# Kernel tuning notes

Hardware: AMD Instinct MI355X
Metric: run time of the kernel (lower is better)

Reference implementation:

```python
import jax, jax.numpy as jnp
import numpy as np

HID = (128, 256, 128)  # nmp_qc NNet hidden layer sizes
D_IN = 256
TARGET = 256


def _mlp_params(key, n_in, n_out, prefix):
    sizes = (n_in,) + HID + (n_out,)
    params = {}
    for i in range(len(sizes) - 1):
        key, k1, k2 = jax.random.split(key, 3)
        fan_in = sizes[i]
        bound = 1.0 / np.sqrt(fan_in)
        params[f"{prefix}_W{i}"] = jax.random.uniform(k1, (sizes[i], sizes[i + 1]), jnp.float32, -bound, bound)
        params[f"{prefix}_b{i}"] = jax.random.uniform(k2, (sizes[i + 1],), jnp.float32, -bound, bound)
    return params, key


def _mlp(x, Ws, bs):
    # ReLU on all layers except the last (linear output), matching NNet
    for i in range(len(Ws) - 1):
        x = jax.nn.relu(x @ Ws[i] + bs[i])
    return x @ Ws[-1] + bs[-1]


def setup_inputs() -> dict:
    key = jax.random.key(0)
    k0, k1, key = jax.random.split(key, 3)
    B, N = 512, 256
    inp = {
        "h0": jax.random.normal(k0, (B, N, D_IN), jnp.float32),
        "hT": jax.random.normal(k1, (B, N, D_IN), jnp.float32),
    }
    gp, key = _mlp_params(key, 2 * D_IN, TARGET, "g")  # gate MLP: concat(h0,hT) -> target
    op, key = _mlp_params(key, D_IN, TARGET, "o")      # value MLP: hT -> target
    inp.update(gp)
    inp.update(op)
    return inp


def reference(h0, hT,
              g_W0, g_b0, g_W1, g_b1, g_W2, g_b2, g_W3, g_b3,
              o_W0, o_b0, o_W1, o_b1, o_W2, o_b2, o_W3, o_b3):
    gWs = (g_W0, g_W1, g_W2, g_W3)
    gbs = (g_b0, g_b1, g_b2, g_b3)
    oWs = (o_W0, o_W1, o_W2, o_W3)
    obs = (o_b0, o_b1, o_b2, o_b3)
    # gate: sigmoid(MLP1([h0; hT])) ; value: MLP2(hT)  -- all [B, N, target]
    gate = jax.nn.sigmoid(_mlp(jnp.concatenate([h0, hT], axis=-1), gWs, gbs))
    val = _mlp(hT, oWs, obs)
    # node validity mask: sum of initial features > 0, matching r_mpnn
    mask = (jnp.sum(h0, axis=-1, keepdims=True) > 0).astype(h0.dtype)  # [B, N, 1]
    return jnp.sum(mask * gate * val, axis=1)  # [B, target]
```

## Files before the change

### kernel.cpp

```cpp
#include <hip/hip_runtime.h>
#include <hip/hip_bf16.h>
#include <stdint.h>


typedef __attribute__((ext_vector_type(8))) short short8_t;
typedef __attribute__((ext_vector_type(16))) float f32x16;

#define ROWS 64
#define NWG  2048

#define PE        (64 * 136)
#define OFF_P     0
#define OFF_A     34816
#define OFF_MASK  52224
#define LDS_TOTAL 52480

__device__ __forceinline__ short f2bf(float f) {
  union { float f; uint32_t u; } v; v.f = f;
  uint32_t r = (v.u + 0x7FFFu + ((v.u >> 16) & 1u)) >> 16;
  return (short)r;
}
__device__ __forceinline__ float bf2f(short b) {
  union { uint32_t u; float f; } v; v.u = ((uint32_t)(uint16_t)b) << 16;
  return v.f;
}

template <int KT16, int KSTEPS, int CT>
__device__ __forceinline__ void gemm32(const short* actin, int Sin,
                                       const short* __restrict__ wsB, int ks0, int cb0,
                                       f32x16 (&acc)[2][CT], int lane) {
  const int n32 = lane & 31, q32 = lane >> 5;
#pragma unroll
  for (int ks = 0; ks < KSTEPS; ++ks) {
    const int kl = ks * 16 + q32 * 8;
    short8_t b[CT];
#pragma unroll
    for (int ct = 0; ct < CT; ++ct)
      b[ct] = *(const short8_t*)(wsB + (((cb0 + ct) * KT16 + ks0 + ks) << 9) + lane * 8);
    short8_t a[2];
#pragma unroll
    for (int rt = 0; rt < 2; ++rt)
      a[rt] = *(const short8_t*)(actin + (rt * 32 + n32) * Sin + kl);
#pragma unroll
    for (int ct = 0; ct < CT; ++ct)
#pragma unroll
      for (int rt = 0; rt < 2; ++rt)
        acc[rt][ct] = __builtin_amdgcn_mfma_f32_32x32x16_bf16(a[rt], b[ct], acc[rt][ct], 0, 0, 0);
  }
}

template <int CT, int ACTF>
__device__ __forceinline__ void epi32(f32x16 (&acc)[2][CT], short* actout, int Sout,
                                      const float* __restrict__ bias, int c0, int n32, int q32) {
#pragma unroll
  for (int ct = 0; ct < CT; ++ct) {
    const int c = c0 + ct * 32 + n32;
    const float bv = bias[c];
#pragma unroll
    for (int rt = 0; rt < 2; ++rt)
#pragma unroll
      for (int reg = 0; reg < 16; ++reg) {
        const int r = rt * 32 + (reg & 3) + 8 * (reg >> 2) + 4 * q32;
        float v = acc[rt][ct][reg] + bv;
        if (ACTF == 1) v = fmaxf(v, 0.f);
        actout[r * Sout + c] = f2bf(v);
      }
  }
}

template <int K, int N, int ACTF>
__device__ __forceinline__ void layer32(const short* actin, int Sin, short* actout, int Sout,
                                        const short* __restrict__ wsB,
                                        const float* __restrict__ bias,
                                        int wv, int lane) {
  constexpr int CT = N / 128;
  const int cb0 = wv * CT;
  const int n32 = lane & 31, q32 = lane >> 5;
  f32x16 acc[2][CT];
#pragma unroll
  for (int rt = 0; rt < 2; ++rt)
#pragma unroll
    for (int ct = 0; ct < CT; ++ct) acc[rt][ct] = (f32x16)(0.f);
  gemm32<K / 16, K / 16, CT>(actin, Sin, wsB, 0, cb0, acc, lane);
  epi32<CT, ACTF>(acc, actout, Sout, bias, cb0 * 32, n32, q32);
}

__device__ __forceinline__ void stage_load(const float* __restrict__ src, int row0, int colbase,
                                           int tid, float4 (&v)[8]) {
  const int c4 = tid & 31, rb = tid >> 5;
#pragma unroll
  for (int it = 0; it < 8; ++it)
    v[it] = *(const float4*)(src + (size_t)(row0 + rb + it * 8) * 256 + colbase + c4 * 4);
}

__device__ __forceinline__ void stage_store(short* Pb, int tid, const float4 (&v)[8],
                                            float* maskacc, int mmode) {
  const int c4 = tid & 31, rb = tid >> 5;
#pragma unroll
  for (int it = 0; it < 8; ++it) {
    const int r = rb + it * 8;
    short4 pk; pk.x = f2bf(v[it].x); pk.y = f2bf(v[it].y); pk.z = f2bf(v[it].z); pk.w = f2bf(v[it].w);
    *(short4*)(Pb + r * 136 + c4 * 4) = pk;
    if (mmode) {
      float s = v[it].x + v[it].y + v[it].z + v[it].w;
      s += __shfl_down(s, 16, 32);
      s += __shfl_down(s, 8, 32);
      s += __shfl_down(s, 4, 32);
      s += __shfl_down(s, 2, 32);
      s += __shfl_down(s, 1, 32);
      if (c4 == 0) {
        if (mmode == 1) maskacc[r] = s; else maskacc[r] += s;
      }
    }
  }
}

template <int NCH, bool MASKA>
__device__ __forceinline__ void stream32(const float* __restrict__ src0,
                                         const float* __restrict__ src1, int splitc,
                                         const short* __restrict__ wsB,
                                         const float* __restrict__ bias,
                                         short* P, short* Aout, float* maskacc,
                                         int row0, int tid, int wv, int lane) {
  constexpr int KT16 = NCH * 8;
  const int n32 = lane & 31, q32 = lane >> 5;
  f32x16 acc[2][1];
  acc[0][0] = (f32x16)(0.f); acc[1][0] = (f32x16)(0.f);
  float4 v[8];
  stage_load(src0, row0, 0, tid, v);
  stage_store(P, tid, v, maskacc, MASKA ? 1 : 0);
  __syncthreads();
#pragma unroll
  for (int kc = 0; kc < NCH; ++kc) {
    if (kc + 1 < NCH) {
      const bool lo = (kc + 1 < splitc);
      stage_load(lo ? src0 : src1, row0, (lo ? kc + 1 : kc + 1 - splitc) * 128, tid, v);
    }
    gemm32<KT16, 8, 1>(P + (kc & 1) * PE, 136, wsB, kc * 8, wv, acc, lane);
    if (kc + 1 < NCH)
      stage_store(P + ((kc + 1) & 1) * PE, tid, v, maskacc, (MASKA && kc + 1 < splitc) ? 2 : 0);
    __syncthreads();
  }
  epi32<1, 1>(acc, Aout, 136, bias, wv * 32, n32, q32);
}

__device__ __forceinline__ void gate_layer(const short* actin, const short* __restrict__ wsB,
                                           const float* __restrict__ bias,
                                           uint32_t (&gate)[2][2][8],
                                           int wv, int lane) {
  const int n32 = lane & 31;
  f32x16 acc[2][2];
#pragma unroll
  for (int rt = 0; rt < 2; ++rt)
#pragma unroll
    for (int ct = 0; ct < 2; ++ct) acc[rt][ct] = (f32x16)(0.f);
  gemm32<8, 8, 2>(actin, 136, wsB, 0, wv * 2, acc, lane);
#pragma unroll
  for (int ct = 0; ct < 2; ++ct) {
    const float bv = bias[wv * 64 + ct * 32 + n32];
#pragma unroll
    for (int rt = 0; rt < 2; ++rt)
#pragma unroll
      for (int p = 0; p < 8; ++p) {
        const float g0 = 1.f / (1.f + __expf(-(acc[rt][ct][2 * p] + bv)));
        const float g1 = 1.f / (1.f + __expf(-(acc[rt][ct][2 * p + 1] + bv)));
        gate[rt][ct][p] = ((uint32_t)(uint16_t)f2bf(g1) << 16) | (uint32_t)(uint16_t)f2bf(g0);
      }
  }
}

__device__ __forceinline__ void final32(const short* actin, const short* __restrict__ wsB,
                                        const float* __restrict__ bias,
                                        const uint32_t (&gate)[2][2][8],
                                        const float* maskacc, float* __restrict__ out,
                                        int row0, int wv, int lane) {
  const int n32 = lane & 31, q32 = lane >> 5;
  f32x16 acc[2][2];
#pragma unroll
  for (int rt = 0; rt < 2; ++rt)
#pragma unroll
    for (int ct = 0; ct < 2; ++ct) acc[rt][ct] = (f32x16)(0.f);
  gemm32<8, 8, 2>(actin, 136, wsB, 0, wv * 2, acc, lane);

  const int b = row0 >> 8;
#pragma unroll
  for (int ct = 0; ct < 2; ++ct) {
    const int c = wv * 64 + ct * 32 + n32;
    const float bv = bias[c];
    float s = 0.f;
#pragma unroll
    for (int rt = 0; rt < 2; ++rt)
#pragma unroll
      for (int p = 0; p < 8; ++p) {
        const int r0 = rt * 32 + ((2 * p) & 3) + 8 * (p >> 1) + 4 * q32;
        const float g0 = bf2f((short)(gate[rt][ct][p] & 0xFFFF));
        const float g1 = bf2f((short)(gate[rt][ct][p] >> 16));
        const float v0 = acc[rt][ct][2 * p] + bv;
        const float v1 = acc[rt][ct][2 * p + 1] + bv;
        if (maskacc[r0] > 0.f)     s += g0 * v0;
        if (maskacc[r0 + 1] > 0.f) s += g1 * v1;
      }
    s += __shfl_down(s, 32);
    if (lane < 32) atomicAdd(out + b * 256 + c, s);
  }
}

__global__ __launch_bounds__(256, 2)
void readout_main(const float* __restrict__ h0, const float* __restrict__ hT,
                  const short* __restrict__ ws,
                  const float* __restrict__ gb0, const float* __restrict__ gb1,
                  const float* __restrict__ gb2, const float* __restrict__ gb3,
                  const float* __restrict__ ob0, const float* __restrict__ ob1,
                  const float* __restrict__ ob2, const float* __restrict__ ob3,
                  float* __restrict__ out) {
  __shared__ __align__(16) char smem[LDS_TOTAL];
  short* P  = (short*)(smem + OFF_P);
  short* B2 = (short*)(smem + OFF_P);
  short* A  = (short*)(smem + OFF_A);
  float* maskacc = (float*)(smem + OFF_MASK);

  const int tid = threadIdx.x, lane = tid & 63, wv = tid >> 6;
  const int row0 = blockIdx.x * ROWS;
  uint32_t gate[2][2][8];

  stream32<4, true>(h0, hT, 2, ws + 0, gb0, P, A, maskacc, row0, tid, wv, lane);
  __syncthreads();
  layer32<128, 256, 1>(A, 136, B2, 264, ws + 65536, gb1, wv, lane);
  __syncthreads();
  layer32<256, 128, 1>(B2, 264, A, 136, ws + 98304, gb2, wv, lane);
  __syncthreads();
  gate_layer(A, ws + 131072, gb3, gate, wv, lane);
  __syncthreads();
  stream32<2, false>(hT, hT, 2, ws + 163840, ob0, P, A, maskacc, row0, tid, wv, lane);
  __syncthreads();
  layer32<128, 256, 1>(A, 136, B2, 264, ws + 196608, ob1, wv, lane);
  __syncthreads();
  layer32<256, 128, 1>(B2, 264, A, 136, ws + 229376, ob2, wv, lane);
  __syncthreads();
  final32(A, ws + 262144, ob3, gate, maskacc, out, row0, wv, lane);
}

__global__ void prep(const float* __restrict__ W0, const float* __restrict__ W1,
                     const float* __restrict__ W2, const float* __restrict__ W3,
                     const float* __restrict__ W4, const float* __restrict__ W5,
                     const float* __restrict__ W6, const float* __restrict__ W7,
                     short* __restrict__ ws, float* __restrict__ out) {
  const int l = blockIdx.y;
  const int le = blockIdx.x * 256 + threadIdx.x;
  if (l == 1) { out[le] = 0.f; out[le + 65536] = 0.f; }
  int K, N, off; const float* W;
  switch (l) {
    case 0:  K = 512; N = 128; off = 0;      W = W0; break;
    case 1:  K = 128; N = 256; off = 65536;  W = W1; break;
    case 2:  K = 256; N = 128; off = 98304;  W = W2; break;
    case 3:  K = 128; N = 256; off = 131072; W = W3; break;
    case 4:  K = 256; N = 128; off = 163840; W = W4; break;
    case 5:  K = 128; N = 256; off = 196608; W = W5; break;
    case 6:  K = 256; N = 128; off = 229376; W = W6; break;
    default: K = 128; N = 256; off = 262144; W = W7; break;
  }
  if (le >= K * N) return;
  const int j = le & 7;
  const int lanei = (le >> 3) & 63;
  const int blk = le >> 9;
  const int kt16 = K >> 4;
  const int ks = blk % kt16, cb = blk / kt16;
  const int n = cb * 32 + (lanei & 31);
  const int k = ks * 16 + (lanei >> 5) * 8 + j;
  ws[off + le] = f2bf(W[k * N + n]);
}

extern "C" void kernel_launch(void* const* d_in, const int* in_sizes, int n_in,
                              void* d_out, int out_size, void* d_ws, size_t ws_size,
                              hipStream_t stream) {
  const float* h0  = (const float*)d_in[0];
  const float* hT  = (const float*)d_in[1];
  const float* gW0 = (const float*)d_in[2];  const float* gb0 = (const float*)d_in[3];
  const float* gW1 = (const float*)d_in[4];  const float* gb1 = (const float*)d_in[5];
  const float* gW2 = (const float*)d_in[6];  const float* gb2 = (const float*)d_in[7];
  const float* gW3 = (const float*)d_in[8];  const float* gb3 = (const float*)d_in[9];
  const float* oW0 = (const float*)d_in[10]; const float* ob0 = (const float*)d_in[11];
  const float* oW1 = (const float*)d_in[12]; const float* ob1 = (const float*)d_in[13];
  const float* oW2 = (const float*)d_in[14]; const float* ob2 = (const float*)d_in[15];
  const float* oW3 = (const float*)d_in[16]; const float* ob3 = (const float*)d_in[17];
  float* out = (float*)d_out;
  short* ws  = (short*)d_ws;

  prep<<<dim3(256, 8), 256, 0, stream>>>(gW0, gW1, gW2, gW3, oW0, oW1, oW2, oW3, ws, out);
  readout_main<<<NWG, 256, 0, stream>>>(h0, hT, ws,
                                        gb0, gb1, gb2, gb3,
                                        ob0, ob1, ob2, ob3, out);
}
```

Before: 468.7 us.

## Split workgroup rows across 8 waves instead of 4

Doubles the threads per workgroup from 256 to 512, so each wave handles one 32-row tile instead of two while keeping the same column split. Streaming loads are spread over twice as many threads, and the launch bounds target more waves per CU to improve latency hiding. In exchange, each B-fragment weight load is now reused across one row tile instead of two, which doubles weight traffic per MFMA. The LDS footprint per 512-thread workgroup limits how many workgroups can be resident on a CU.

```diff
diff --git a/kernel.cpp b/kernel.cpp
--- a/kernel.cpp
+++ b/kernel.cpp
@@ -8,6 +8,7 @@
 
 #define ROWS 64
 #define NWG  2048
+#define NTHR 512
 
 #define PE        (64 * 136)
 #define OFF_P     0
@@ -28,7 +29,7 @@
 template <int KT16, int KSTEPS, int CT>
 __device__ __forceinline__ void gemm32(const short* actin, int Sin,
                                        const short* __restrict__ wsB, int ks0, int cb0,
-                                       f32x16 (&acc)[2][CT], int lane) {
+                                       f32x16 (&acc)[CT], int lane) {
   const int n32 = lane & 31, q32 = lane >> 5;
 #pragma unroll
   for (int ks = 0; ks < KSTEPS; ++ks) {
@@ -37,34 +38,27 @@
 #pragma unroll
     for (int ct = 0; ct < CT; ++ct)
       b[ct] = *(const short8_t*)(wsB + (((cb0 + ct) * KT16 + ks0 + ks) << 9) + lane * 8);
-    short8_t a[2];
-#pragma unroll
-    for (int rt = 0; rt < 2; ++rt)
-      a[rt] = *(const short8_t*)(actin + (rt * 32 + n32) * Sin + kl);
+    const short8_t a = *(const short8_t*)(actin + n32 * Sin + kl);
 #pragma unroll
     for (int ct = 0; ct < CT; ++ct)
-#pragma unroll
-      for (int rt = 0; rt < 2; ++rt)
-        acc[rt][ct] = __builtin_amdgcn_mfma_f32_32x32x16_bf16(a[rt], b[ct], acc[rt][ct], 0, 0, 0);
+      acc[ct] = __builtin_amdgcn_mfma_f32_32x32x16_bf16(a, b[ct], acc[ct], 0, 0, 0);
   }
 }
 
 template <int CT, int ACTF>
-__device__ __forceinline__ void epi32(f32x16 (&acc)[2][CT], short* actout, int Sout,
+__device__ __forceinline__ void epi32(f32x16 (&acc)[CT], short* actout, int Sout,
                                       const float* __restrict__ bias, int c0, int n32, int q32) {
 #pragma unroll
   for (int ct = 0; ct < CT; ++ct) {
     const int c = c0 + ct * 32 + n32;
     const float bv = bias[c];
 #pragma unroll
-    for (int rt = 0; rt < 2; ++rt)
-#pragma unroll
-      for (int reg = 0; reg < 16; ++reg) {
-        const int r = rt * 32 + (reg & 3) + 8 * (reg >> 2) + 4 * q32;
-        float v = acc[rt][ct][reg] + bv;
-        if (ACTF == 1) v = fmaxf(v, 0.f);
-        actout[r * Sout + c] = f2bf(v);
-      }
+    for (int reg = 0; reg < 16; ++reg) {
+      const int r = (reg & 3) + 8 * (reg >> 2) + 4 * q32;
+      float v = acc[ct][reg] + bv;
+      if (ACTF == 1) v = fmaxf(v, 0.f);
+      actout[r * Sout + c] = f2bf(v);
+    }
   }
 }
 
@@ -72,33 +66,31 @@
 __device__ __forceinline__ void layer32(const short* actin, int Sin, short* actout, int Sout,
                                         const short* __restrict__ wsB,
                                         const float* __restrict__ bias,
-                                        int wv, int lane) {
+                                        int wq, int lane) {
   constexpr int CT = N / 128;
-  const int cb0 = wv * CT;
-  const int n32 = lane & 31, q32 = lane >> 5;
-  f32x16 acc[2][CT];
-#pragma unroll
-  for (int rt = 0; rt < 2; ++rt)
-#pragma unroll
-    for (int ct = 0; ct < CT; ++ct) acc[rt][ct] = (f32x16)(0.f);
+  const int cb0 = wq * CT;
+  const int n32 = lane & 31, q32 = lane >> 5;
+  f32x16 acc[CT];
+#pragma unroll
+  for (int ct = 0; ct < CT; ++ct) acc[ct] = (f32x16)(0.f);
   gemm32<K / 16, K / 16, CT>(actin, Sin, wsB, 0, cb0, acc, lane);
   epi32<CT, ACTF>(acc, actout, Sout, bias, cb0 * 32, n32, q32);
 }
 
 __device__ __forceinline__ void stage_load(const float* __restrict__ src, int row0, int colbase,
-                                           int tid, float4 (&v)[8]) {
+                                           int tid, float4 (&v)[4]) {
   const int c4 = tid & 31, rb = tid >> 5;
 #pragma unroll
-  for (int it = 0; it < 8; ++it)
-    v[it] = *(const float4*)(src + (size_t)(row0 + rb + it * 8) * 256 + colbase + c4 * 4);
-}
-
-__device__ __forceinline__ void stage_store(short* Pb, int tid, const float4 (&v)[8],
+  for (int it = 0; it < 4; ++it)
+    v[it] = *(const float4*)(src + (size_t)(row0 + rb + it * 16) * 256 + colbase + c4 * 4);
+}
+
+__device__ __forceinline__ void stage_store(short* Pb, int tid, const float4 (&v)[4],
                                             float* maskacc, int mmode) {
   const int c4 = tid & 31, rb = tid >> 5;
 #pragma unroll
-  for (int it = 0; it < 8; ++it) {
-    const int r = rb + it * 8;
+  for (int it = 0; it < 4; ++it) {
+    const int r = rb + it * 16;
     short4 pk; pk.x = f2bf(v[it].x); pk.y = f2bf(v[it].y); pk.z = f2bf(v[it].z); pk.w = f2bf(v[it].w);
     *(short4*)(Pb + r * 136 + c4 * 4) = pk;
     if (mmode) {
@@ -121,12 +113,12 @@
                                          const short* __restrict__ wsB,
                                          const float* __restrict__ bias,
                                          short* P, short* Aout, float* maskacc,
-                                         int row0, int tid, int wv, int lane) {
+                                         int row0, int tid, int wq, int rowsh, int lane) {
   constexpr int KT16 = NCH * 8;
   const int n32 = lane & 31, q32 = lane >> 5;
-  f32x16 acc[2][1];
-  acc[0][0] = (f32x16)(0.f); acc[1][0] = (f32x16)(0.f);
-  float4 v[8];
+  f32x16 acc[1];
+  acc[0] = (f32x16)(0.f);
+  float4 v[4];
   stage_load(src0, row0, 0, tid, v);
   stage_store(P, tid, v, maskacc, MASKA ? 1 : 0);
   __syncthreads();
@@ -136,76 +128,66 @@
       const bool lo = (kc + 1 < splitc);
       stage_load(lo ? src0 : src1, row0, (lo ? kc + 1 : kc + 1 - splitc) * 128, tid, v);
     }
-    gemm32<KT16, 8, 1>(P + (kc & 1) * PE, 136, wsB, kc * 8, wv, acc, lane);
+    gemm32<KT16, 8, 1>(P + (kc & 1) * PE + rowsh, 136, wsB, kc * 8, wq, acc, lane);
     if (kc + 1 < NCH)
       stage_store(P + ((kc + 1) & 1) * PE, tid, v, maskacc, (MASKA && kc + 1 < splitc) ? 2 : 0);
     __syncthreads();
   }
-  epi32<1, 1>(acc, Aout, 136, bias, wv * 32, n32, q32);
+  epi32<1, 1>(acc, Aout, 136, bias, wq * 32, n32, q32);
 }
 
 __device__ __forceinline__ void gate_layer(const short* actin, const short* __restrict__ wsB,
                                            const float* __restrict__ bias,
-                                           uint32_t (&gate)[2][2][8],
-                                           int wv, int lane) {
+                                           uint32_t (&gate)[2][8],
+                                           int wq, int lane) {
   const int n32 = lane & 31;
-  f32x16 acc[2][2];
-#pragma unroll
-  for (int rt = 0; rt < 2; ++rt)
-#pragma unroll
-    for (int ct = 0; ct < 2; ++ct) acc[rt][ct] = (f32x16)(0.f);
-  gemm32<8, 8, 2>(actin, 136, wsB, 0, wv * 2, acc, lane);
+  f32x16 acc[2];
+  acc[0] = (f32x16)(0.f); acc[1] = (f32x16)(0.f);
+  gemm32<8, 8, 2>(actin, 136, wsB, 0, wq * 2, acc, lane);
 #pragma unroll
   for (int ct = 0; ct < 2; ++ct) {
-    const float bv = bias[wv * 64 + ct * 32 + n32];
-#pragma unroll
-    for (int rt = 0; rt < 2; ++rt)
-#pragma unroll
-      for (int p = 0; p < 8; ++p) {
-        const float g0 = 1.f / (1.f + __expf(-(acc[rt][ct][2 * p] + bv)));
-        const float g1 = 1.f / (1.f + __expf(-(acc[rt][ct][2 * p + 1] + bv)));
-        gate[rt][ct][p] = ((uint32_t)(uint16_t)f2bf(g1) << 16) | (uint32_t)(uint16_t)f2bf(g0);
-      }
+    const float bv = bias[wq * 64 + ct * 32 + n32];
+#pragma unroll
+    for (int p = 0; p < 8; ++p) {
+      const float g0 = 1.f / (1.f + __expf(-(acc[ct][2 * p] + bv)));
+      const float g1 = 1.f / (1.f + __expf(-(acc[ct][2 * p + 1] + bv)));
+      gate[ct][p] = ((uint32_t)(uint16_t)f2bf(g1) << 16) | (uint32_t)(uint16_t)f2bf(g0);
+    }
   }
 }
 
 __device__ __forceinline__ void final32(const short* actin, const short* __restrict__ wsB,
                                         const float* __restrict__ bias,
-                                        const uint32_t (&gate)[2][2][8],
+                                        const uint32_t (&gate)[2][8],
                                         const float* maskacc, float* __restrict__ out,
-                                        int row0, int wv, int lane) {
-  const int n32 = lane & 31, q32 = lane >> 5;
-  f32x16 acc[2][2];
-#pragma unroll
-  for (int rt = 0; rt < 2; ++rt)
-#pragma unroll
-    for (int ct = 0; ct < 2; ++ct) acc[rt][ct] = (f32x16)(0.f);
-  gemm32<8, 8, 2>(actin, 136, wsB, 0, wv * 2, acc, lane);
+                                        int row0, int wq, int lane) {
+  const int n32 = lane & 31, q32 = lane >> 5;
+  f32x16 acc[2];
+  acc[0] = (f32x16)(0.f); acc[1] = (f32x16)(0.f);
+  gemm32<8, 8, 2>(actin, 136, wsB, 0, wq * 2, acc, lane);
 
   const int b = row0 >> 8;
 #pragma unroll
   for (int ct = 0; ct < 2; ++ct) {
-    const int c = wv * 64 + ct * 32 + n32;
+    const int c = wq * 64 + ct * 32 + n32;
     const float bv = bias[c];
     float s = 0.f;
 #pragma unroll
-    for (int rt = 0; rt < 2; ++rt)
-#pragma unroll
-      for (int p = 0; p < 8; ++p) {
-        const int r0 = rt * 32 + ((2 * p) & 3) + 8 * (p >> 1) + 4 * q32;
-        const float g0 = bf2f((short)(gate[rt][ct][p] & 0xFFFF));
-        const float g1 = bf2f((short)(gate[rt][ct][p] >> 16));
-        const float v0 = acc[rt][ct][2 * p] + bv;
-        const float v1 = acc[rt][ct][2 * p + 1] + bv;
-        if (maskacc[r0] > 0.f)     s += g0 * v0;
-        if (maskacc[r0 + 1] > 0.f) s += g1 * v1;
-      }
+    for (int p = 0; p < 8; ++p) {
+      const int r0 = ((2 * p) & 3) + 8 * (p >> 1) + 4 * q32;
+      const float g0 = bf2f((short)(gate[ct][p] & 0xFFFF));
+      const float g1 = bf2f((short)(gate[ct][p] >> 16));
+      const float v0 = acc[ct][2 * p] + bv;
+      const float v1 = acc[ct][2 * p + 1] + bv;
+      if (maskacc[r0] > 0.f)     s += g0 * v0;
+      if (maskacc[r0 + 1] > 0.f) s += g1 * v1;
+    }
     s += __shfl_down(s, 32);
     if (lane < 32) atomicAdd(out + b * 256 + c, s);
   }
 }
 
-__global__ __launch_bounds__(256, 2)
+__global__ __launch_bounds__(NTHR, 6)
 void readout_main(const float* __restrict__ h0, const float* __restrict__ hT,
                   const short* __restrict__ ws,
                   const float* __restrict__ gb0, const float* __restrict__ gb1,
@@ -220,24 +202,28 @@
   float* maskacc = (float*)(smem + OFF_MASK);
 
   const int tid = threadIdx.x, lane = tid & 63, wv = tid >> 6;
+  const int wq = wv & 3;
+  const int rhalf = wv >> 2;
+  const int rsh136 = rhalf * 32 * 136;
+  const int rsh264 = rhalf * 32 * 264;
   const int row0 = blockIdx.x * ROWS;
-  uint32_t gate[2][2][8];
-
-  stream32<4, true>(h0, hT, 2, ws + 0, gb0, P, A, maskacc, row0, tid, wv, lane);
-  __syncthreads();
-  layer32<128, 256, 1>(A, 136, B2, 264, ws + 65536, gb1, wv, lane);
-  __syncthreads();
-  layer32<256, 128, 1>(B2, 264, A, 136, ws + 98304, gb2, wv, lane);
-  __syncthreads();
-  gate_layer(A, ws + 131072, gb3, gate, wv, lane);
-  __syncthreads();
-  stream32<2, false>(hT, hT, 2, ws + 163840, ob0, P, A, maskacc, row0, tid, wv, lane);
-  __syncthreads();
-  layer32<128, 256, 1>(A, 136, B2, 264, ws + 196608, ob1, wv, lane);
-  __syncthreads();
-  layer32<256, 128, 1>(B2, 264, A, 136, ws + 229376, ob2, wv, lane);
-  __syncthreads();
-  final32(A, ws + 262144, ob3, gate, maskacc, out, row0, wv, lane);
+  uint32_t gate[2][8];
+
+  stream32<4, true>(h0, hT, 2, ws + 0, gb0, P, A + rsh136, maskacc, row0, tid, wq, rsh136, lane);
+  __syncthreads();
+  layer32<128, 256, 1>(A + rsh136, 136, B2 + rsh264, 264, ws + 65536, gb1, wq, lane);
+  __syncthreads();
+  layer32<256, 128, 1>(B2 + rsh264, 264, A + rsh136, 136, ws + 98304, gb2, wq, lane);
+  __syncthreads();
+  gate_layer(A + rsh136, ws + 131072, gb3, gate, wq, lane);
+  __syncthreads();
+  stream32<2, false>(hT, hT, 2, ws + 163840, ob0, P, A + rsh136, maskacc, row0, tid, wq, rsh136, lane);
+  __syncthreads();
+  layer32<128, 256, 1>(A + rsh136, 136, B2 + rsh264, 264, ws + 196608, ob1, wq, lane);
+  __syncthreads();
+  layer32<256, 128, 1>(B2 + rsh264, 264, A + rsh136, 136, ws + 229376, ob2, wq, lane);
+  __syncthreads();
+  final32(A + rsh136, ws + 262144, ob3, gate, maskacc + rhalf * 32, out, row0, wq, lane);
 }
 
 __global__ void prep(const float* __restrict__ W0, const float* __restrict__ W1,
@@ -287,7 +273,7 @@
   short* ws  = (short*)d_ws;
 
   prep<<<dim3(256, 8), 256, 0, stream>>>(gW0, gW1, gW2, gW3, oW0, oW1, oW2, oW3, ws, out);
-  readout_main<<<NWG, 256, 0, stream>>>(h0, hT, ws,
-                                        gb0, gb1, gb2, gb3,
-                                        ob0, ob1, ob2, ob3, out);
-}
+  readout_main<<<NWG, NTHR, 0, stream>>>(h0, hT, ws,
+                                         gb0, gb1, gb2, gb3,
+                                         ob0, ob1, ob2, ob3, out);
+}
```

New measurement: 429.7 us. 1.09x faster.
